# Kernel tuning notes

Measured on AMD Instinct MI355X. Metric: run time of the kernel, lower is better.

## Reference

```python
import jax, jax.numpy as jnp
import numpy as np

B = 8192          # batch of scenes
H = 20            # human_num
O = 10            # other_robot_num
IN = 13           # input_dim
SELF = 6          # self_state_dim
AG = IN - SELF    # agent_state_dim = 7
E1, E2 = 256, 128 # wr_dims / wh_dims
HID = 32          # hardcoded hidden_channels in Graphgnn
FIN = 128         # final_state_dim
P1, P2, P3 = 256, 128, 1  # planning_dims
NE = 8            # number of hetero edge types
# edge-type index convention:
# 0 robot->human, 1 human->robot, 2 other->robot, 3 robot->other,
# 4 other->human, 5 human->other, 6 human->human, 7 other->other


def setup_inputs() -> dict:
    key = jax.random.key(0)
    ks = iter(jax.random.split(key, 40))
    def nrm(shape, scale=0.05):
        return jax.random.normal(next(ks), shape, jnp.float32) * scale
    inp = {}
    inp["state"] = jax.random.normal(next(ks), (B, H + O, IN), jnp.float32)
    inp["dropout"] = 0  # unused by forward (kept for signature fidelity)
    # w_r: SELF -> E1 -> E2 (last_relu=True)
    inp["wr_W0"] = nrm((SELF, E1)); inp["wr_b0"] = nrm((E1,))
    inp["wr_W1"] = nrm((E1, E2));   inp["wr_b1"] = nrm((E2,))
    # w_h: AG -> E1 -> E2
    inp["wh_W0"] = nrm((AG, E1));   inp["wh_b0"] = nrm((E1,))
    inp["wh_W1"] = nrm((E1, E2));   inp["wh_b1"] = nrm((E2,))
    # w_o: AG -> E1 -> E2
    inp["wo_W0"] = nrm((AG, E1));   inp["wo_b0"] = nrm((E1,))
    inp["wo_W1"] = nrm((E1, E2));   inp["wo_b1"] = nrm((E2,))
    # per-edge-type GraphConv params (PyG GraphConv: lin_rel has bias, lin_root has none)
    inp["c1_relW"]  = nrm((NE, E2, HID)); inp["c1_relb"]  = nrm((NE, HID))
    inp["c1_rootW"] = nrm((NE, E2, HID))
    inp["c2_relW"]  = nrm((NE, HID, FIN)); inp["c2_relb"]  = nrm((NE, FIN))
    inp["c2_rootW"] = nrm((NE, HID, FIN))
    # value_net: FIN -> P1 -> P2 -> P3 (no final relu)
    inp["v_W0"] = nrm((FIN, P1)); inp["v_b0"] = nrm((P1,))
    inp["v_W1"] = nrm((P1, P2));  inp["v_b1"] = nrm((P2,))
    inp["v_W2"] = nrm((P2, P3));  inp["v_b2"] = nrm((P3,))
    return inp


def _mlp2(x, W0, b0, W1, b1, last_relu):
    h = jax.nn.relu(x @ W0 + b0)
    h = h @ W1 + b1
    return jax.nn.relu(h) if last_relu else h


def _hetero_conv(xr, xh, xo, relW, relb, rootW):
    # xr: [B,1,D], xh: [B,H,D], xo: [B,O,D]
    # GraphConv per edge type: out_dst = lin_root(x_dst) + lin_rel(sum of src messages)
    # graph is complete bipartite (sence) / complete-minus-self (affect),
    # so aggregations are closed-form sums.
    lin  = lambda x, i: jnp.einsum('bnd,do->bno', x, relW[i]) + relb[i]
    root = lambda x, i: jnp.einsum('bnd,do->bno', x, rootW[i])
    sh = xh.sum(axis=1, keepdims=True)  # [B,1,D] sum over humans
    so = xo.sum(axis=1, keepdims=True)  # [B,1,D] sum over other robots
    # robot receives: human->robot (1), other->robot (2)
    out_r = lin(sh, 1) + root(xr, 1) + lin(so, 2) + root(xr, 2)
    # human receives: robot->human (0), other->human (4), human->human (6)
    out_h = (lin(xr, 0) + root(xh, 0)
             + lin(so, 4) + root(xh, 4)
             + lin(sh - xh, 6) + root(xh, 6))
    # other receives: robot->other (3), human->other (5), other->other (7)
    out_o = (lin(xr, 3) + root(xo, 3)
             + lin(sh, 5) + root(xo, 5)
             + lin(so - xo, 7) + root(xo, 7))
    return out_r, out_h, out_o


def reference(state, dropout,
              wr_W0, wr_b0, wr_W1, wr_b1,
              wh_W0, wh_b0, wh_W1, wh_b1,
              wo_W0, wo_b0, wo_W1, wo_b1,
              c1_relW, c1_relb, c1_rootW,
              c2_relW, c2_relb, c2_rootW,
              v_W0, v_b0, v_W1, v_b1, v_W2, v_b2):
    self_state = state[:, 0, :SELF]          # [B, SELF]
    human_states = state[:, :H, SELF:]       # [B, H, AG]
    other_states = state[:, H:, SELF:]       # [B, O, AG]
    er = _mlp2(self_state, wr_W0, wr_b0, wr_W1, wr_b1, True)[:, None, :]  # [B,1,E2]
    eh = _mlp2(human_states, wh_W0, wh_b0, wh_W1, wh_b1, True)            # [B,H,E2]
    eo = _mlp2(other_states, wo_W0, wo_b0, wo_W1, wo_b1, True)            # [B,O,E2]
    r, h, o = _hetero_conv(er, eh, eo, c1_relW, c1_relb, c1_rootW)
    r, h, o = jax.nn.relu(r), jax.nn.relu(h), jax.nn.relu(o)
    r, h, o = _hetero_conv(r, h, o, c2_relW, c2_relb, c2_rootW)
    r = jax.nn.relu(r)
    hr = r[:, 0, :]                           # robot node per scene, [B, FIN]
    v = jax.nn.relu(hr @ v_W0 + v_b0)
    v = jax.nn.relu(v @ v_W1 + v_b1)
    v = v @ v_W2 + v_b2                       # [B, 1]
    return v
```

## Files before the change

### kernel.cpp

```cpp
#include <hip/hip_runtime.h>
#include <hip/hip_bf16.h>
#include <stdint.h>

#define BATCH 8192
#define NSTATE 30
#define DIN 13
#define E1 256
#define E2 128

typedef short bf16x8 __attribute__((ext_vector_type(8)));
typedef float f32x4 __attribute__((ext_vector_type(4)));

__device__ __forceinline__ unsigned short f2b(float f) {
    unsigned u = __float_as_uint(f);
    u += 0x7FFFu + ((u >> 16) & 1u);
    return (unsigned short)(u >> 16);
}
__device__ __forceinline__ float b2f(unsigned short b) {
    return __uint_as_float((unsigned)b << 16);
}
__device__ __forceinline__ unsigned pack2(float a, float b) {
    return ((unsigned)f2b(fmaxf(b, 0.f)) << 16) | f2b(fmaxf(a, 0.f));
}
__device__ __forceinline__ unsigned pack2n(float a, float b) {
    return ((unsigned)f2b(b) << 16) | f2b(a);
}

__device__ __forceinline__ float wcat_val(int k, int m, const float* relW, const float* rootW) {
    int part = k >> 7, c = k & 127, grp = m >> 5, mm = m & 31;
    int off = c * 32 + mm;
    if (part == 0) return (grp == 0) ? rootW[4096 + off] + rootW[8192 + off]
                        : (grp == 1) ? relW[off] : relW[3*4096 + off];
    if (part == 1) return (grp == 0) ? relW[1*4096 + off]
                        : (grp == 1) ? relW[6*4096 + off] : relW[5*4096 + off];
    return (grp == 0) ? relW[2*4096 + off]
         : (grp == 1) ? relW[4*4096 + off] : relW[7*4096 + off];
}
__device__ __forceinline__ float wc2_val(int k, int n, const float* relW, const float* rootW) {
    int grp = k >> 5, kk = k & 31;
    int off = kk * 128 + n;
    if (grp == 0) return rootW[4096 + off] + rootW[8192 + off];
    if (grp == 1) return relW[4096 + off];
    return relW[8192 + off];
}

__global__ void k_prep(const float* __restrict__ c1_relW, const float* __restrict__ c1_relb,
                       const float* __restrict__ c1_rootW,
                       const float* __restrict__ c2_relW, const float* __restrict__ c2_relb,
                       const float* __restrict__ c2_rootW,
                       const float* __restrict__ wh_W0, const float* __restrict__ wh_W1,
                       const float* __restrict__ wo_W0, const float* __restrict__ wo_W1,
                       const float* __restrict__ wr_W0, const float* __restrict__ wr_W1,
                       const float* __restrict__ v_W0, const float* __restrict__ v_W1,
                       float* __restrict__ bcat, float* __restrict__ bc2,
                       unsigned short* __restrict__ W0b_h, unsigned short* __restrict__ W0b_o,
                       unsigned short* __restrict__ W0b_r,
                       unsigned short* __restrict__ W1f_h, unsigned short* __restrict__ W1f_o,
                       unsigned short* __restrict__ W1f_r,
                       unsigned short* __restrict__ Mf_h, unsigned short* __restrict__ Mf_o,
                       unsigned short* __restrict__ Wcatf, unsigned short* __restrict__ Wc2f,
                       unsigned short* __restrict__ vW0f, unsigned short* __restrict__ vW1f)
{
    int gid = blockIdx.x * blockDim.x + threadIdx.x;
    int gsz = gridDim.x * blockDim.x;

    for (int i = gid; i < 96; i += gsz) {
        int grp = i >> 5, mm = i & 31;
        float v;
        if (grp == 0)      v = c1_relb[32 + mm] + c1_relb[64 + mm];
        else if (grp == 1) v = c1_relb[mm] + c1_relb[128 + mm] + c1_relb[192 + mm];
        else               v = c1_relb[96 + mm] + c1_relb[160 + mm] + c1_relb[224 + mm];
        bcat[i] = v;
    }
    for (int i = gid; i < 128; i += gsz) bc2[i] = c2_relb[128 + i] + c2_relb[256 + i];

    for (int i = gid; i < 2048; i += gsz) {
        int n = i >> 3, j = i & 7;
        W0b_h[i] = (j < 7) ? f2b(wh_W0[j * 256 + n]) : 0;
        W0b_o[i] = (j < 7) ? f2b(wo_W0[j * 256 + n]) : 0;
        W0b_r[i] = (j < 6) ? f2b(wr_W0[j * 256 + n]) : 0;
    }
    for (int i = gid; i < 32768; i += gsz) {
        int j = i & 7, l = (i >> 3) & 63, nt = (i >> 9) & 7, ks = i >> 12;
        int k = ks * 32 + (l >> 4) * 8 + j;
        int n = nt * 16 + (l & 15);
        W1f_h[i] = f2b(wh_W1[k * 128 + n]);
        W1f_o[i] = f2b(wo_W1[k * 128 + n]);
        W1f_r[i] = f2b(wr_W1[k * 128 + n]);
    }
    for (int i = gid; i < 4096; i += gsz) {
        int j = i & 7, l = (i >> 3) & 63, nt = (i >> 9) & 1, ks = i >> 10;
        int k = ks * 32 + (l >> 4) * 8 + j;
        int n = nt * 16 + (l & 15);
        int i0 = k * 32 + n;
        Mf_h[i] = f2b(c1_rootW[i0] + c1_rootW[4*4096 + i0] + c1_rootW[6*4096 + i0] - c1_relW[6*4096 + i0]);
        Mf_o[i] = f2b(c1_rootW[3*4096 + i0] + c1_rootW[5*4096 + i0] + c1_rootW[7*4096 + i0] - c1_relW[7*4096 + i0]);
    }
    for (int i = gid; i < 36864; i += gsz) {
        int j = i & 7, l = (i >> 3) & 63, rem = i >> 9;
        int nt = rem % 6, ks = rem / 6;
        int k = ks * 32 + (l >> 4) * 8 + j;
        int n = nt * 16 + (l & 15);
        Wcatf[i] = f2b(wcat_val(k, n, c1_relW, c1_rootW));
    }
    for (int i = gid; i < 12288; i += gsz) {
        int j = i & 7, l = (i >> 3) & 63, rem = i >> 9;
        int nt = rem & 7, ks = rem >> 3;
        int k = ks * 32 + (l >> 4) * 8 + j;
        int n = nt * 16 + (l & 15);
        Wc2f[i] = f2b(wc2_val(k, n, c2_relW, c2_rootW));
    }
    for (int i = gid; i < 32768; i += gsz) {
        int j = i & 7, l = (i >> 3) & 63, rem = i >> 9;
        int nt = rem & 15, ks = rem >> 4;
        int k = ks * 32 + (l >> 4) * 8 + j;
        int n = nt * 16 + (l & 15);
        vW0f[i] = f2b(v_W0[k * 256 + n]);
    }
    for (int i = gid; i < 32768; i += gsz) {
        int j = i & 7, l = (i >> 3) & 63, rem = i >> 9;
        int nt = rem & 7, ks = rem >> 3;
        int k = ks * 32 + (l >> 4) * 8 + j;
        int n = nt * 16 + (l & 15);
        vW1f[i] = f2b(v_W1[k * 128 + n]);
    }
}

#define SM_W0   0
#define SM_MF   4096
#define SM_W1   12288
#define SM_HS   77824
#define SM_SZ   (77824 + 8 * 16 * 264 * 2)

template<int NPB, int NODE0, int INOFF, int INDIM, bool TAIL>
__device__ __forceinline__ void mlp_blockE(
    int blkrow0, const float* __restrict__ state,
    const unsigned short* __restrict__ W0b_g, const float* __restrict__ b0,
    const unsigned short* __restrict__ W1f_g, const float* __restrict__ b1,
    const unsigned short* __restrict__ Mf_g,
    unsigned short* __restrict__ tR, float* __restrict__ sumB,
    unsigned short* __restrict__ eR, char* smem)
{
    unsigned short* W0s = (unsigned short*)(smem + SM_W0);
    unsigned short* Mfs = (unsigned short*)(smem + SM_MF);
    unsigned short* W1s = (unsigned short*)(smem + SM_W1);

    const int t = threadIdx.x;
    const int lane = t & 63;
    const int w = t >> 6;
    const int l15 = lane & 15;
    const int quad = lane >> 4;
    const int R0 = blkrow0 + w * 128;
    unsigned short* hw = (unsigned short*)(smem + SM_HS) + w * (16 * 264);
    unsigned short* ew = hw;

    if (t < 256) ((uint4*)W0s)[t] = ((const uint4*)W0b_g)[t];
    #pragma unroll
    for (int i = 0; i < 8; ++i)
        ((uint4*)W1s)[t + 512 * i] = ((const uint4*)W1f_g)[t + 512 * i];
    if constexpr (TAIL)
        ((uint4*)Mfs)[t] = ((const uint4*)Mf_g)[t];

    f32x4 b0r[16], b1r[8];
    #pragma unroll
    for (int nt = 0; nt < 16; ++nt) {
        float4 bb = *(const float4*)(b0 + nt * 16 + quad * 4);
        b0r[nt] = (f32x4){bb.x, bb.y, bb.z, bb.w};
    }
    #pragma unroll
    for (int nt = 0; nt < 8; ++nt) {
        float4 bb = *(const float4*)(b1 + nt * 16 + quad * 4);
        b1r[nt] = (f32x4){bb.x, bb.y, bb.z, bb.w};
    }
    __syncthreads();

    float s0 = 0.f, s1 = 0.f;
    int bcur = R0 / NPB;

    for (int sub = 0; sub < 8; ++sub) {
        const int wrow0 = R0 + sub * 16;

        bf16x8 bx = {};
        if (quad == 0) {
            int grow = wrow0 + l15;
            int b = grow / NPB;
            int n = grow - b * NPB + NODE0;
            const float* xp = state + ((size_t)b * NSTATE + n) * DIN + INOFF;
            #pragma unroll
            for (int j = 0; j < INDIM; ++j)
                bx[j] = (short)f2b(xp[j]);
        }

        #pragma unroll
        for (int nt = 0; nt < 16; ++nt) {
            bf16x8 aw = {};
            if (quad == 0)
                aw = *(const bf16x8*)(W0s + (nt * 16 + l15) * 8);
            f32x4 c = b0r[nt];
            c = __builtin_amdgcn_mfma_f32_16x16x32_bf16(aw, bx, c, 0, 0, 0);
            uint2 pv = {pack2(c[0], c[1]), pack2(c[2], c[3])};
            *(uint2*)(hw + l15 * 264 + nt * 16 + quad * 4) = pv;
        }

        f32x4 acc[8];
        #pragma unroll
        for (int nt = 0; nt < 8; ++nt) acc[nt] = b1r[nt];
        #pragma unroll
        for (int ks = 0; ks < 8; ++ks) {
            bf16x8 bh = *(const bf16x8*)(hw + l15 * 264 + ks * 32 + quad * 8);
            #pragma unroll
            for (int nt = 0; nt < 8; ++nt) {
                bf16x8 aw = *(const bf16x8*)(W1s + ((ks * 8 + nt) * 64 + lane) * 8);
                acc[nt] = __builtin_amdgcn_mfma_f32_16x16x32_bf16(aw, bh, acc[nt], 0, 0, 0);
            }
        }

        if constexpr (TAIL) {
            __asm__ __volatile__("s_waitcnt lgkmcnt(0)" ::: "memory");
            #pragma unroll
            for (int nt = 0; nt < 8; ++nt) {
                uint2 pv = {pack2(acc[nt][0], acc[nt][1]), pack2(acc[nt][2], acc[nt][3])};
                *(uint2*)(ew + l15 * 136 + nt * 16 + quad * 4) = pv;
            }

            f32x4 tacc[2] = {{0.f,0.f,0.f,0.f},{0.f,0.f,0.f,0.f}};
            #pragma unroll
            for (int ks = 0; ks < 4; ++ks) {
                bf16x8 ae = *(const bf16x8*)(ew + l15 * 136 + ks * 32 + quad * 8);
                #pragma unroll
                for (int nt = 0; nt < 2; ++nt) {
                    bf16x8 bm = *(const bf16x8*)(Mfs + ((ks * 2 + nt) * 64 + lane) * 8);
                    tacc[nt] = __builtin_amdgcn_mfma_f32_16x16x32_bf16(bm, ae, tacc[nt], 0, 0, 0);
                }
            }
            #pragma unroll
            for (int nt = 0; nt < 2; ++nt) {
                uint2 pv = {pack2n(tacc[nt][0], tacc[nt][1]), pack2n(tacc[nt][2], tacc[nt][3])};
                *(uint2*)(tR + (size_t)(wrow0 + l15) * 32 + nt * 16 + quad * 4) = pv;
            }

            #pragma unroll
            for (int r = 0; r < 16; ++r) {
                int b = (wrow0 + r) / NPB;
                if (b != bcur) {
                    bool interior = (bcur * NPB >= R0) && ((bcur + 1) * NPB <= R0 + 128);
                    float* dst = sumB + (size_t)bcur * 128 + 2 * lane;
                    if (interior) { dst[0] = s0; dst[1] = s1; }
                    else { atomicAdd(dst, s0); atomicAdd(dst + 1, s1); }
                    s0 = 0.f; s1 = 0.f; bcur = b;
                }
                unsigned v = *(const unsigned*)(ew + r * 136 + lane * 2);
                s0 += b2f((unsigned short)v);
                s1 += b2f((unsigned short)(v >> 16));
            }
            if (sub == 7) {
                bool interior = (bcur * NPB >= R0) && ((bcur + 1) * NPB <= R0 + 128);
                float* dst = sumB + (size_t)bcur * 128 + 2 * lane;
                if (interior) { dst[0] = s0; dst[1] = s1; }
                else { atomicAdd(dst, s0); atomicAdd(dst + 1, s1); }
            }
        } else {
            #pragma unroll
            for (int nt = 0; nt < 8; ++nt) {
                uint2 pv = {pack2(acc[nt][0], acc[nt][1]), pack2(acc[nt][2], acc[nt][3])};
                *(uint2*)(eR + (size_t)(wrow0 + l15) * 128 + nt * 16 + quad * 4) = pv;
            }
        }
        __asm__ __volatile__("" ::: "memory");
    }
}

__global__ __launch_bounds__(512, 2) void k_mlpE(
    const float* __restrict__ state,
    const unsigned short* __restrict__ W0b_h, const float* __restrict__ b0_h,
    const unsigned short* __restrict__ W1f_h, const float* __restrict__ b1_h,
    const unsigned short* __restrict__ Mf_h, unsigned short* __restrict__ tR_h,
    float* __restrict__ shB,
    const unsigned short* __restrict__ W0b_o, const float* __restrict__ b0_o,
    const unsigned short* __restrict__ W1f_o, const float* __restrict__ b1_o,
    const unsigned short* __restrict__ Mf_o, unsigned short* __restrict__ tR_o,
    float* __restrict__ soB,
    const unsigned short* __restrict__ W0b_r, const float* __restrict__ b0_r,
    const unsigned short* __restrict__ W1f_r, const float* __restrict__ b1_r,
    unsigned short* __restrict__ eR)
{
    __shared__ __align__(16) char smem[SM_SZ];
    int bid = blockIdx.x;
    if (bid < 160)
        mlp_blockE<20, 0, 6, 7, true>(bid * 1024, state, W0b_h, b0_h, W1f_h, b1_h,
                                      Mf_h, tR_h, shB, nullptr, smem);
    else if (bid < 240)
        mlp_blockE<10, 20, 6, 7, true>((bid - 160) * 1024, state, W0b_o, b0_o, W1f_o, b1_o,
                                       Mf_o, tR_o, soB, nullptr, smem);
    else
        mlp_blockE<1, 0, 0, 6, false>((bid - 240) * 1024, state, W0b_r, b0_r, W1f_r, b1_r,
                                      nullptr, nullptr, nullptr, eR, smem);
}

__global__ __launch_bounds__(256, 2) void k_tail(
    const unsigned short* __restrict__ eR,
    const float* __restrict__ shB, const float* __restrict__ soB,
    const unsigned short* __restrict__ tR_h, const unsigned short* __restrict__ tR_o,
    const unsigned short* __restrict__ Wcatf, const float* __restrict__ bcat,
    const unsigned short* __restrict__ Wc2f, const float* __restrict__ bc2,
    const unsigned short* __restrict__ vW0f, const float* __restrict__ vb0,
    const unsigned short* __restrict__ vW1f, const float* __restrict__ vb1,
    const float* __restrict__ vW2, const float* __restrict__ vb2,
    float* __restrict__ out)
{
    __shared__ __align__(16) char sm[66048];
    unsigned short* Ub  = (unsigned short*)(sm);
    unsigned short* V1b = (unsigned short*)(sm);
    unsigned short* Vb  = (unsigned short*)(sm + 25600);
    float* chL          = (float*)(sm + 32256);
    float* coL          = (float*)(sm + 36352);
    unsigned short* Hb  = (unsigned short*)(sm + 40448);
    float* V2b          = (float*)(sm + 49152);

    const int t = threadIdx.x, lane = t & 63, w = t >> 6;
    const int l15 = lane & 15, quad = lane >> 4;
    const int b0 = blockIdx.x * 32;
    const int mt = w >> 1, nh = w & 1;
    const int rowb = mt * 16 + quad * 4;

    {
        int b = t >> 3, q = t & 7;
        const uint4* src = (const uint4*)(eR + (size_t)(b0 + b) * 128 + q * 16);
        uint4 v0 = src[0], v1 = src[1];
        uint4* dst = (uint4*)(Ub + b * 400 + q * 16);
        dst[0] = v0; dst[1] = v1;
    }
    for (int idx = t; idx < 8192; idx += 256) {
        int kk = idx >> 5, b = idx & 31;
        float v = (kk < 128) ? shB[(size_t)(b0 + b) * 128 + kk]
                             : soB[(size_t)(b0 + b) * 128 + kk - 128];
        Ub[b * 400 + 128 + kk] = f2b(v);
    }
    __syncthreads();

    {
        const int ntg = nh * 3;
        f32x4 acc[3];
        #pragma unroll
        for (int q = 0; q < 3; ++q) {
            float bias = bcat[(ntg + q) * 16 + l15];
            acc[q] = (f32x4){bias, bias, bias, bias};
        }
        #pragma unroll
        for (int ks = 0; ks < 12; ++ks) {
            bf16x8 a = *(const bf16x8*)(Ub + (mt * 16 + l15) * 400 + ks * 32 + quad * 8);
            #pragma unroll
            for (int q = 0; q < 3; ++q) {
                bf16x8 bw = *(const bf16x8*)(Wcatf + ((ks * 6 + ntg + q) * 64 + lane) * 8);
                acc[q] = __builtin_amdgcn_mfma_f32_16x16x32_bf16(a, bw, acc[q], 0, 0, 0);
            }
        }
        #pragma unroll
        for (int q = 0; q < 3; ++q) {
            int n = (ntg + q) * 16 + l15;
            #pragma unroll
            for (int reg = 0; reg < 4; ++reg) {
                float v = acc[q][reg];
                int b = mt * 16 + quad * 4 + reg;
                if (n < 32)      Vb[b * 104 + n] = f2b(fmaxf(v, 0.f));
                else if (n < 64) chL[b * 32 + (n - 32)] = v;
                else             coL[b * 32 + (n - 64)] = v;
            }
        }
    }
    __syncthreads();

    for (int idx = t; idx < 1024; idx += 256) {
        int b = idx >> 5, m = idx & 31;
        float ch = chL[b * 32 + m];
        const unsigned short* p = tR_h + (size_t)(b0 + b) * 20 * 32 + m;
        float s = 0.f;
        #pragma unroll
        for (int n = 0; n < 20; ++n) s += fmaxf(ch + b2f(p[n * 32]), 0.f);
        Vb[b * 104 + 32 + m] = f2b(s);
        float co = coL[b * 32 + m];
        const unsigned short* p2 = tR_o + (size_t)(b0 + b) * 10 * 32 + m;
        float s2 = 0.f;
        #pragma unroll
        for (int n = 0; n < 10; ++n) s2 += fmaxf(co + b2f(p2[n * 32]), 0.f);
        Vb[b * 104 + 64 + m] = f2b(s2);
    }
    __syncthreads();

    {
        const int ntg = nh * 4;
        f32x4 acc[4];
        #pragma unroll
        for (int q = 0; q < 4; ++q) {
            float bias = bc2[(ntg + q) * 16 + l15];
            acc[q] = (f32x4){bias, bias, bias, bias};
        }
        #pragma unroll
        for (int ks = 0; ks < 3; ++ks) {
            bf16x8 a = *(const bf16x8*)(Vb + (mt * 16 + l15) * 104 + ks * 32 + quad * 8);
            #pragma unroll
            for (int q = 0; q < 4; ++q) {
                bf16x8 bw = *(const bf16x8*)(Wc2f + ((ks * 8 + ntg + q) * 64 + lane) * 8);
                acc[q] = __builtin_amdgcn_mfma_f32_16x16x32_bf16(a, bw, acc[q], 0, 0, 0);
            }
        }
        #pragma unroll
        for (int q = 0; q < 4; ++q)
            #pragma unroll
            for (int reg = 0; reg < 4; ++reg)
                Hb[(rowb + reg) * 136 + (ntg + q) * 16 + l15] = f2b(fmaxf(acc[q][reg], 0.f));
    }
    __syncthreads();

    {
        const int ntg = nh * 8;
        f32x4 acc[8];
        #pragma unroll
        for (int q = 0; q < 8; ++q) {
            float bias = vb0[(ntg + q) * 16 + l15];
            acc[q] = (f32x4){bias, bias, bias, bias};
        }
        #pragma unroll
        for (int ks = 0; ks < 4; ++ks) {
            bf16x8 a = *(const bf16x8*)(Hb + (mt * 16 + l15) * 136 + ks * 32 + quad * 8);
            #pragma unroll
            for (int q = 0; q < 8; ++q) {
                bf16x8 bw = *(const bf16x8*)(vW0f + ((ks * 16 + ntg + q) * 64 + lane) * 8);
                acc[q] = __builtin_amdgcn_mfma_f32_16x16x32_bf16(a, bw, acc[q], 0, 0, 0);
            }
        }
        #pragma unroll
        for (int q = 0; q < 8; ++q)
            #pragma unroll
            for (int reg = 0; reg < 4; ++reg)
                V1b[(rowb + reg) * 264 + (ntg + q) * 16 + l15] = f2b(fmaxf(acc[q][reg], 0.f));
    }
    __syncthreads();

    {
        const int ntg = nh * 4;
        f32x4 acc[4];
        #pragma unroll
        for (int q = 0; q < 4; ++q) {
            float bias = vb1[(ntg + q) * 16 + l15];
            acc[q] = (f32x4){bias, bias, bias, bias};
        }
        #pragma unroll
        for (int ks = 0; ks < 8; ++ks) {
            bf16x8 a = *(const bf16x8*)(V1b + (mt * 16 + l15) * 264 + ks * 32 + quad * 8);
            #pragma unroll
            for (int q = 0; q < 4; ++q) {
                bf16x8 bw = *(const bf16x8*)(vW1f + ((ks * 8 + ntg + q) * 64 + lane) * 8);
                acc[q] = __builtin_amdgcn_mfma_f32_16x16x32_bf16(a, bw, acc[q], 0, 0, 0);
            }
        }
        #pragma unroll
        for (int q = 0; q < 4; ++q)
            #pragma unroll
            for (int reg = 0; reg < 4; ++reg)
                V2b[(rowb + reg) * 132 + (ntg + q) * 16 + l15] = fmaxf(acc[q][reg], 0.f);
    }
    __syncthreads();

    {
        int b = t >> 3, j = t & 7;
        float v = 0.f;
        #pragma unroll
        for (int k = 0; k < 16; ++k)
            v = fmaf(V2b[b * 132 + j * 16 + k], vW2[j * 16 + k], v);
        v += __shfl_down(v, 4, 8);
        v += __shfl_down(v, 2, 8);
        v += __shfl_down(v, 1, 8);
        if (j == 0) out[b0 + b] = v + vb2[0];
    }
}

extern "C" void kernel_launch(void* const* d_in, const int* in_sizes, int n_in,
                              void* d_out, int out_size, void* d_ws, size_t ws_size,
                              hipStream_t stream)
{
    const float* state   = (const float*)d_in[0];
    const float* wr_W0   = (const float*)d_in[2];
    const float* wr_b0   = (const float*)d_in[3];
    const float* wr_W1   = (const float*)d_in[4];
    const float* wr_b1   = (const float*)d_in[5];
    const float* wh_W0   = (const float*)d_in[6];
    const float* wh_b0   = (const float*)d_in[7];
    const float* wh_W1   = (const float*)d_in[8];
    const float* wh_b1   = (const float*)d_in[9];
    const float* wo_W0   = (const float*)d_in[10];
    const float* wo_b0   = (const float*)d_in[11];
    const float* wo_W1   = (const float*)d_in[12];
    const float* wo_b1   = (const float*)d_in[13];
    const float* c1_relW = (const float*)d_in[14];
    const float* c1_relb = (const float*)d_in[15];
    const float* c1_rootW= (const float*)d_in[16];
    const float* c2_relW = (const float*)d_in[17];
    const float* c2_relb = (const float*)d_in[18];
    const float* c2_rootW= (const float*)d_in[19];
    const float* v_W0    = (const float*)d_in[20];
    const float* v_b0    = (const float*)d_in[21];
    const float* v_W1    = (const float*)d_in[22];
    const float* v_b1    = (const float*)d_in[23];
    const float* v_W2    = (const float*)d_in[24];
    const float* v_b2    = (const float*)d_in[25];

    char* ws = (char*)d_ws;
    size_t off = 0;
    auto alloc = [&](size_t bytes) -> char* {
        char* p = ws + off;
        off = (off + bytes + 255) & ~(size_t)255;
        return p;
    };
    float* shB  = (float*)alloc((size_t)BATCH * 128 * 4);
    float* soB  = (float*)alloc((size_t)BATCH * 128 * 4);
    unsigned short* tR_h = (unsigned short*)alloc((size_t)163840 * 32 * 2);
    unsigned short* tR_o = (unsigned short*)alloc((size_t)81920 * 32 * 2);
    unsigned short* eR   = (unsigned short*)alloc((size_t)BATCH * 128 * 2);
    float* bcat = (float*)alloc(96 * 4);
    float* bc2  = (float*)alloc(128 * 4);
    unsigned short* W0b_h = (unsigned short*)alloc(2048 * 2);
    unsigned short* W0b_o = (unsigned short*)alloc(2048 * 2);
    unsigned short* W0b_r = (unsigned short*)alloc(2048 * 2);
    unsigned short* W1f_h = (unsigned short*)alloc(32768 * 2);
    unsigned short* W1f_o = (unsigned short*)alloc(32768 * 2);
    unsigned short* W1f_r = (unsigned short*)alloc(32768 * 2);
    unsigned short* Mf_h  = (unsigned short*)alloc(4096 * 2);
    unsigned short* Mf_o  = (unsigned short*)alloc(4096 * 2);
    unsigned short* Wcatf = (unsigned short*)alloc(36864 * 2);
    unsigned short* Wc2f  = (unsigned short*)alloc(12288 * 2);
    unsigned short* vW0f  = (unsigned short*)alloc(32768 * 2);
    unsigned short* vW1f  = (unsigned short*)alloc(32768 * 2);
    (void)ws_size; (void)in_sizes; (void)n_in; (void)out_size;

    hipMemsetAsync(shB, 0, (size_t)2 * BATCH * 128 * 4, stream);

    k_prep<<<256, 256, 0, stream>>>(c1_relW, c1_relb, c1_rootW, c2_relW, c2_relb, c2_rootW,
                                    wh_W0, wh_W1, wo_W0, wo_W1, wr_W0, wr_W1, v_W0, v_W1,
                                    bcat, bc2, W0b_h, W0b_o, W0b_r, W1f_h, W1f_o, W1f_r,
                                    Mf_h, Mf_o, Wcatf, Wc2f, vW0f, vW1f);

    k_mlpE<<<248, 512, 0, stream>>>(state,
                                    W0b_h, wh_b0, W1f_h, wh_b1, Mf_h, tR_h, shB,
                                    W0b_o, wo_b0, W1f_o, wo_b1, Mf_o, tR_o, soB,
                                    W0b_r, wr_b0, W1f_r, wr_b1, eR);

    k_tail<<<256, 256, 0, stream>>>(eR, shB, soB, tR_h, tR_o,
                                    Wcatf, bcat, Wc2f, bc2, vW0f, v_b0, vW1f, v_b1,
                                    v_W2, v_b2, (float*)d_out);
}
```

Baseline: 185.0 us.

## Halve tail-kernel scenes per block and stage MLP biases in LDS

Result: faster. 173.7 us (-6.1%).

```diff
diff --git a/kernel.cpp b/kernel.cpp
--- a/kernel.cpp
+++ b/kernel.cpp
@@ -129,8 +129,10 @@
 #define SM_W0   0
 #define SM_MF   4096
 #define SM_W1   12288
-#define SM_HS   77824
-#define SM_SZ   (77824 + 8 * 16 * 264 * 2)
+#define SM_B0   77824
+#define SM_B1   78848
+#define SM_HS   79360
+#define SM_SZ   (79360 + 8 * 16 * 264 * 2)
 
 template<int NPB, int NODE0, int INOFF, int INDIM, bool TAIL>
 __device__ __forceinline__ void mlp_blockE(
@@ -144,6 +146,8 @@
     unsigned short* W0s = (unsigned short*)(smem + SM_W0);
     unsigned short* Mfs = (unsigned short*)(smem + SM_MF);
     unsigned short* W1s = (unsigned short*)(smem + SM_W1);
+    float* b0s          = (float*)(smem + SM_B0);
+    float* b1s          = (float*)(smem + SM_B1);
 
     const int t = threadIdx.x;
     const int lane = t & 63;
@@ -154,24 +158,13 @@
     unsigned short* hw = (unsigned short*)(smem + SM_HS) + w * (16 * 264);
     unsigned short* ew = hw;
 
-    if (t < 256) ((uint4*)W0s)[t] = ((const uint4*)W0b_g)[t];
+    if (t < 256) { ((uint4*)W0s)[t] = ((const uint4*)W0b_g)[t]; b0s[t] = b0[t]; }
+    if (t >= 256 && t < 384) b1s[t - 256] = b1[t - 256];
     #pragma unroll
     for (int i = 0; i < 8; ++i)
         ((uint4*)W1s)[t + 512 * i] = ((const uint4*)W1f_g)[t + 512 * i];
     if constexpr (TAIL)
         ((uint4*)Mfs)[t] = ((const uint4*)Mf_g)[t];
-
-    f32x4 b0r[16], b1r[8];
-    #pragma unroll
-    for (int nt = 0; nt < 16; ++nt) {
-        float4 bb = *(const float4*)(b0 + nt * 16 + quad * 4);
-        b0r[nt] = (f32x4){bb.x, bb.y, bb.z, bb.w};
-    }
-    #pragma unroll
-    for (int nt = 0; nt < 8; ++nt) {
-        float4 bb = *(const float4*)(b1 + nt * 16 + quad * 4);
-        b1r[nt] = (f32x4){bb.x, bb.y, bb.z, bb.w};
-    }
     __syncthreads();
 
     float s0 = 0.f, s1 = 0.f;
@@ -196,7 +189,8 @@
             bf16x8 aw = {};
             if (quad == 0)
                 aw = *(const bf16x8*)(W0s + (nt * 16 + l15) * 8);
-            f32x4 c = b0r[nt];
+            float4 bb = *(const float4*)(b0s + nt * 16 + quad * 4);
+            f32x4 c = {bb.x, bb.y, bb.z, bb.w};
             c = __builtin_amdgcn_mfma_f32_16x16x32_bf16(aw, bx, c, 0, 0, 0);
             uint2 pv = {pack2(c[0], c[1]), pack2(c[2], c[3])};
             *(uint2*)(hw + l15 * 264 + nt * 16 + quad * 4) = pv;
@@ -204,7 +198,10 @@
 
         f32x4 acc[8];
         #pragma unroll
-        for (int nt = 0; nt < 8; ++nt) acc[nt] = b1r[nt];
+        for (int nt = 0; nt < 8; ++nt) {
+            float4 bb = *(const float4*)(b1s + nt * 16 + quad * 4);
+            acc[nt] = (f32x4){bb.x, bb.y, bb.z, bb.w};
+        }
         #pragma unroll
         for (int ks = 0; ks < 8; ++ks) {
             bf16x8 bh = *(const bf16x8*)(hw + l15 * 264 + ks * 32 + quad * 8);
@@ -308,69 +305,54 @@
     const float* __restrict__ vW2, const float* __restrict__ vb2,
     float* __restrict__ out)
 {
-    __shared__ __align__(16) char sm[66048];
+    __shared__ __align__(16) char sm[33024];
     unsigned short* Ub  = (unsigned short*)(sm);
     unsigned short* V1b = (unsigned short*)(sm);
-    unsigned short* Vb  = (unsigned short*)(sm + 25600);
-    float* chL          = (float*)(sm + 32256);
-    float* coL          = (float*)(sm + 36352);
-    unsigned short* Hb  = (unsigned short*)(sm + 40448);
-    float* V2b          = (float*)(sm + 49152);
+    unsigned short* Vb  = (unsigned short*)(sm + 12800);
+    float* chL          = (float*)(sm + 16128);
+    float* coL          = (float*)(sm + 18176);
+    unsigned short* Hb  = (unsigned short*)(sm + 20224);
+    float* V2b          = (float*)(sm + 24576);
 
     const int t = threadIdx.x, lane = t & 63, w = t >> 6;
     const int l15 = lane & 15, quad = lane >> 4;
-    const int b0 = blockIdx.x * 32;
-    const int mt = w >> 1, nh = w & 1;
-    const int rowb = mt * 16 + quad * 4;
+    const int b0 = blockIdx.x * 16;
+    const int rowb = quad * 4;
 
     {
-        int b = t >> 3, q = t & 7;
-        const uint4* src = (const uint4*)(eR + (size_t)(b0 + b) * 128 + q * 16);
-        uint4 v0 = src[0], v1 = src[1];
-        uint4* dst = (uint4*)(Ub + b * 400 + q * 16);
-        dst[0] = v0; dst[1] = v1;
-    }
-    for (int idx = t; idx < 8192; idx += 256) {
-        int kk = idx >> 5, b = idx & 31;
+        int b = t >> 4, q = t & 15;
+        ((uint4*)(Ub + b * 400))[q] = ((const uint4*)(eR + (size_t)(b0 + b) * 128))[q];
+    }
+    for (int idx = t; idx < 4096; idx += 256) {
+        int b = idx >> 8, kk = idx & 255;
         float v = (kk < 128) ? shB[(size_t)(b0 + b) * 128 + kk]
                              : soB[(size_t)(b0 + b) * 128 + kk - 128];
         Ub[b * 400 + 128 + kk] = f2b(v);
     }
     __syncthreads();
 
-    {
-        const int ntg = nh * 3;
-        f32x4 acc[3];
-        #pragma unroll
-        for (int q = 0; q < 3; ++q) {
-            float bias = bcat[(ntg + q) * 16 + l15];
-            acc[q] = (f32x4){bias, bias, bias, bias};
-        }
+    for (int nt = w; nt < 6; nt += 4) {
+        float bias = bcat[nt * 16 + l15];
+        f32x4 acc = {bias, bias, bias, bias};
         #pragma unroll
         for (int ks = 0; ks < 12; ++ks) {
-            bf16x8 a = *(const bf16x8*)(Ub + (mt * 16 + l15) * 400 + ks * 32 + quad * 8);
-            #pragma unroll
-            for (int q = 0; q < 3; ++q) {
-                bf16x8 bw = *(const bf16x8*)(Wcatf + ((ks * 6 + ntg + q) * 64 + lane) * 8);
-                acc[q] = __builtin_amdgcn_mfma_f32_16x16x32_bf16(a, bw, acc[q], 0, 0, 0);
-            }
-        }
-        #pragma unroll
-        for (int q = 0; q < 3; ++q) {
-            int n = (ntg + q) * 16 + l15;
-            #pragma unroll
-            for (int reg = 0; reg < 4; ++reg) {
-                float v = acc[q][reg];
-                int b = mt * 16 + quad * 4 + reg;
-                if (n < 32)      Vb[b * 104 + n] = f2b(fmaxf(v, 0.f));
-                else if (n < 64) chL[b * 32 + (n - 32)] = v;
-                else             coL[b * 32 + (n - 64)] = v;
-            }
-        }
-    }
-    __syncthreads();
-
-    for (int idx = t; idx < 1024; idx += 256) {
+            bf16x8 a = *(const bf16x8*)(Ub + l15 * 400 + ks * 32 + quad * 8);
+            bf16x8 bw = *(const bf16x8*)(Wcatf + ((ks * 6 + nt) * 64 + lane) * 8);
+            acc = __builtin_amdgcn_mfma_f32_16x16x32_bf16(a, bw, acc, 0, 0, 0);
+        }
+        int n = nt * 16 + l15;
+        #pragma unroll
+        for (int reg = 0; reg < 4; ++reg) {
+            float v = acc[reg];
+            int b = rowb + reg;
+            if (n < 32)      Vb[b * 104 + n] = f2b(fmaxf(v, 0.f));
+            else if (n < 64) chL[b * 32 + (n - 32)] = v;
+            else             coL[b * 32 + (n - 64)] = v;
+        }
+    }
+    __syncthreads();
+
+    for (int idx = t; idx < 512; idx += 256) {
         int b = idx >> 5, m = idx & 31;
         float ch = chL[b * 32 + m];
         const unsigned short* p = tR_h + (size_t)(b0 + b) * 20 * 32 + m;
@@ -388,81 +370,91 @@
     __syncthreads();
 
     {
-        const int ntg = nh * 4;
+        f32x4 acc[2];
+        #pragma unroll
+        for (int q = 0; q < 2; ++q) {
+            int nt = w + q * 4;
+            float bias = bc2[nt * 16 + l15];
+            acc[q] = (f32x4){bias, bias, bias, bias};
+        }
+        #pragma unroll
+        for (int ks = 0; ks < 3; ++ks) {
+            bf16x8 a = *(const bf16x8*)(Vb + l15 * 104 + ks * 32 + quad * 8);
+            #pragma unroll
+            for (int q = 0; q < 2; ++q) {
+                int nt = w + q * 4;
+                bf16x8 bw = *(const bf16x8*)(Wc2f + ((ks * 8 + nt) * 64 + lane) * 8);
+                acc[q] = __builtin_amdgcn_mfma_f32_16x16x32_bf16(a, bw, acc[q], 0, 0, 0);
+            }
+        }
+        #pragma unroll
+        for (int q = 0; q < 2; ++q) {
+            int nt = w + q * 4;
+            #pragma unroll
+            for (int reg = 0; reg < 4; ++reg)
+                Hb[(rowb + reg) * 136 + nt * 16 + l15] = f2b(fmaxf(acc[q][reg], 0.f));
+        }
+    }
+    __syncthreads();
+
+    {
         f32x4 acc[4];
         #pragma unroll
         for (int q = 0; q < 4; ++q) {
-            float bias = bc2[(ntg + q) * 16 + l15];
+            int nt = w + q * 4;
+            float bias = vb0[nt * 16 + l15];
             acc[q] = (f32x4){bias, bias, bias, bias};
         }
         #pragma unroll
-        for (int ks = 0; ks < 3; ++ks) {
-            bf16x8 a = *(const bf16x8*)(Vb + (mt * 16 + l15) * 104 + ks * 32 + quad * 8);
+        for (int ks = 0; ks < 4; ++ks) {
+            bf16x8 a = *(const bf16x8*)(Hb + l15 * 136 + ks * 32 + quad * 8);
             #pragma unroll
             for (int q = 0; q < 4; ++q) {
-                bf16x8 bw = *(const bf16x8*)(Wc2f + ((ks * 8 + ntg + q) * 64 + lane) * 8);
+                int nt = w + q * 4;
+                bf16x8 bw = *(const bf16x8*)(vW0f + ((ks * 16 + nt) * 64 + lane) * 8);
                 acc[q] = __builtin_amdgcn_mfma_f32_16x16x32_bf16(a, bw, acc[q], 0, 0, 0);
             }
         }
-        #pragma unroll
-        for (int q = 0; q < 4; ++q)
+        __syncthreads();
+        #pragma unroll
+        for (int q = 0; q < 4; ++q) {
+            int nt = w + q * 4;
             #pragma unroll
             for (int reg = 0; reg < 4; ++reg)
-                Hb[(rowb + reg) * 136 + (ntg + q) * 16 + l15] = f2b(fmaxf(acc[q][reg], 0.f));
+                V1b[(rowb + reg) * 264 + nt * 16 + l15] = f2b(fmaxf(acc[q][reg], 0.f));
+        }
     }
     __syncthreads();
 
     {
-        const int ntg = nh * 8;
-        f32x4 acc[8];
-        #pragma unroll
-        for (int q = 0; q < 8; ++q) {
-            float bias = vb0[(ntg + q) * 16 + l15];
+        f32x4 acc[2];
+        #pragma unroll
+        for (int q = 0; q < 2; ++q) {
+            int nt = w + q * 4;
+            float bias = vb1[nt * 16 + l15];
             acc[q] = (f32x4){bias, bias, bias, bias};
         }
         #pragma unroll
-        for (int ks = 0; ks < 4; ++ks) {
-            bf16x8 a = *(const bf16x8*)(Hb + (mt * 16 + l15) * 136 + ks * 32 + quad * 8);
-            #pragma unroll
-            for (int q = 0; q < 8; ++q) {
-                bf16x8 bw = *(const bf16x8*)(vW0f + ((ks * 16 + ntg + q) * 64 + lane) * 8);
+        for (int ks = 0; ks < 8; ++ks) {
+            bf16x8 a = *(const bf16x8*)(V1b + l15 * 264 + ks * 32 + quad * 8);
+            #pragma unroll
+            for (int q = 0; q < 2; ++q) {
+                int nt = w + q * 4;
+                bf16x8 bw = *(const bf16x8*)(vW1f + ((ks * 8 + nt) * 64 + lane) * 8);
                 acc[q] = __builtin_amdgcn_mfma_f32_16x16x32_bf16(a, bw, acc[q], 0, 0, 0);
             }
         }
         #pragma unroll
-        for (int q = 0; q < 8; ++q)
+        for (int q = 0; q < 2; ++q) {
+            int nt = w + q * 4;
             #pragma unroll
             for (int reg = 0; reg < 4; ++reg)
-                V1b[(rowb + reg) * 264 + (ntg + q) * 16 + l15] = f2b(fmaxf(acc[q][reg], 0.f));
-    }
-    __syncthreads();
-
-    {
-        const int ntg = nh * 4;
-        f32x4 acc[4];
-        #pragma unroll
-        for (int q = 0; q < 4; ++q) {
-            float bias = vb1[(ntg + q) * 16 + l15];
-            acc[q] = (f32x4){bias, bias, bias, bias};
-        }
-        #pragma unroll
-        for (int ks = 0; ks < 8; ++ks) {
-            bf16x8 a = *(const bf16x8*)(V1b + (mt * 16 + l15) * 264 + ks * 32 + quad * 8);
-            #pragma unroll
-            for (int q = 0; q < 4; ++q) {
-                bf16x8 bw = *(const bf16x8*)(vW1f + ((ks * 8 + ntg + q) * 64 + lane) * 8);
-                acc[q] = __builtin_amdgcn_mfma_f32_16x16x32_bf16(a, bw, acc[q], 0, 0, 0);
-            }
-        }
-        #pragma unroll
-        for (int q = 0; q < 4; ++q)
-            #pragma unroll
-            for (int reg = 0; reg < 4; ++reg)
-                V2b[(rowb + reg) * 132 + (ntg + q) * 16 + l15] = fmaxf(acc[q][reg], 0.f);
-    }
-    __syncthreads();
-
-    {
+                V2b[(rowb + reg) * 132 + nt * 16 + l15] = fmaxf(acc[q][reg], 0.f);
+        }
+    }
+    __syncthreads();
+
+    if (t < 128) {
         int b = t >> 3, j = t & 7;
         float v = 0.f;
         #pragma unroll
@@ -545,7 +537,7 @@
                                     W0b_o, wo_b0, W1f_o, wo_b1, Mf_o, tR_o, soB,
                                     W0b_r, wr_b0, W1f_r, wr_b1, eR);
 
-    k_tail<<<256, 256, 0, stream>>>(eR, shB, soB, tR_h, tR_o,
+    k_tail<<<512, 256, 0, stream>>>(eR, shB, soB, tR_h, tR_o,
                                     Wcatf, bcat, Wc2f, bc2, vW0f, v_b0, vW1f, v_b1,
                                     v_W2, v_b2, (float*)d_out);
 }
```
